# Performance work log

Hardware: AMD Instinct MI355X
Metric: run time of the kernel (lower is better)

## Reference

```python
import jax, jax.numpy as jnp
from jax import lax
import numpy as np

B, N, F_IN, T = 8, 2048, 2, 12
K, F_CHEV, F_TIME = 3, 64, 64
LN_EPS = 1e-5


def _cheb_polys(key):
    # random symmetric row-normalized 'scaled Laplacian' proxy, then Chebyshev recurrence
    A = jax.random.uniform(key, (N, N), dtype=jnp.float32)
    A = (A + A.T) * 0.5
    A = A / A.sum(axis=1, keepdims=True)
    L = A - jnp.eye(N, dtype=jnp.float32)  # eigenvalues roughly in [-1, 1]
    Ts = [jnp.eye(N, dtype=jnp.float32), L]
    for _ in range(2, K):
        Ts.append(2.0 * L @ Ts[-1] - Ts[-2])
    return jnp.stack(Ts[:K])  # (K, N, N)


def setup_inputs() -> dict:
    key = jax.random.key(0)
    ks = jax.random.split(key, 20)
    g = lambda i, s: jax.random.normal(ks[i], s, dtype=jnp.float32)
    xav = lambda i, s: g(i, s) * np.sqrt(2.0 / (s[-2] + s[-1]))
    return {
        "x": g(0, (B, N, F_IN, T)),
        "cheb": _cheb_polys(ks[1]),
        "Theta": xav(2, (K, F_IN, F_CHEV)),
        # temporal attention params
        "U1": g(3, (N,)), "U2": xav(4, (F_IN, N)), "U3": g(5, (F_IN,)),
        "be": g(6, (1, T, T)) * 0.1, "Ve": xav(7, (T, T)),
        # spatial attention params
        "W1": g(8, (T,)), "W2": xav(9, (F_IN, T)), "W3": g(10, (F_IN,)),
        "bs": g(11, (1, N, N)) * 0.1, "Vs": xav(12, (N, N)),
        # convs + layernorm
        "tconv_w": g(13, (F_TIME, F_CHEV, 1, 3)) * np.sqrt(2.0 / (F_CHEV * 3 + F_TIME)),
        "tconv_b": jax.random.uniform(ks[14], (F_TIME,), dtype=jnp.float32),
        "rconv_w": g(15, (F_TIME, F_IN, 1, 1)) * np.sqrt(2.0 / (F_IN + F_TIME)),
        "rconv_b": jax.random.uniform(ks[16], (F_TIME,), dtype=jnp.float32),
        "ln_g": jnp.ones((F_TIME,), jnp.float32),
        "ln_b": jnp.zeros((F_TIME,), jnp.float32),
    }


def _forward(x, cheb, Theta, U1, U2, U3, be, Ve, W1, W2, W3, bs, Vs,
             tconv_w, tconv_b, rconv_w, rconv_b, ln_g, ln_b):
    b, n, f, t = x.shape
    # ---- temporal attention: (B,T,T) ----
    lhs_t = jnp.einsum('bnft,n->btf', x, U1) @ U2          # (B,T,N)
    rhs_t = jnp.einsum('f,bnft->bnt', U3, x)               # (B,N,T)
    prod_t = jnp.einsum('btn,bnu->btu', lhs_t, rhs_t)      # (B,T,T)
    E = jnp.einsum('tu,buv->btv', Ve, jax.nn.sigmoid(prod_t + be))
    E = jax.nn.softmax(E, axis=1)
    # apply temporal attention
    x_TAt = (x.reshape(b, n * f, t) @ E).reshape(b, n, f, t)
    # ---- spatial attention: (B,N,N) ----
    lhs_s = jnp.einsum('bnft,t->bnf', x_TAt, W1) @ W2      # (B,N,T)
    rhs_s = jnp.einsum('f,bnft->btn', W3, x_TAt)           # (B,T,N)
    prod_s = jnp.einsum('bnt,btm->bnm', lhs_s, rhs_s)      # (B,N,N)
    S = jnp.einsum('mn,bnp->bmp', Vs, jax.nn.sigmoid(prod_s + bs))
    S = jax.nn.softmax(S, axis=1)
    # ---- Chebyshev graph conv with spatial attention (vectorized over k, t) ----
    # rhs[b,k,n,f,t] = sum_m (cheb[k,m,n] * S[b,m,n]) * x[b,m,f,t]
    rhs = jnp.einsum('kmn,bmn,bmft->bknft', cheb, S, x)
    gcn = jax.nn.relu(jnp.einsum('bknft,kfo->bnot', rhs, Theta))  # (B,N,F_chev,T)
    # ---- time conv (1x3, pad 1 along T) + 1x1 residual conv ----
    dn = ('NCHW', 'OIHW', 'NCHW')
    tc = lax.conv_general_dilated(gcn.transpose(0, 2, 1, 3), tconv_w, (1, 1),
                                  ((0, 0), (1, 1)), dimension_numbers=dn)
    tc = tc + tconv_b[None, :, None, None]                 # (B,F_time,N,T)
    res = lax.conv_general_dilated(x.transpose(0, 2, 1, 3), rconv_w, (1, 1),
                                   ((0, 0), (0, 0)), dimension_numbers=dn)
    res = res + rconv_b[None, :, None, None]
    y = jax.nn.relu(res + tc).transpose(0, 3, 2, 1)        # (B,T,N,F_time)
    mu = y.mean(-1, keepdims=True)
    var = jnp.mean((y - mu) ** 2, axis=-1, keepdims=True)
    y = (y - mu) * lax.rsqrt(var + LN_EPS) * ln_g + ln_b
    return y.transpose(0, 2, 3, 1)                          # (B,N,F_time,T)


def reference(x, cheb, Theta, U1, U2, U3, be, Ve, W1, W2, W3, bs, Vs,
              tconv_w, tconv_b, rconv_w, rconv_b, ln_g, ln_b):
    return _forward(x, cheb, Theta, U1, U2, U3, be, Ve, W1, W2, W3, bs, Vs,
                    tconv_w, tconv_b, rconv_w, rconv_b, ln_g, ln_b)
```

## Files before the change

kernel.cpp:

```cpp
#include <hip/hip_runtime.h>
#include <cstdint>
#include <cstddef>

#define NB 8
#define NN 2048
#define MCV 32

using bf16x8 = __attribute__((ext_vector_type(8))) __bf16;
using f32x4  = __attribute__((ext_vector_type(4))) float;

__device__ __forceinline__ float bf2f(unsigned short u) {
  union { unsigned int i; float f; } v; v.i = ((unsigned int)u) << 16; return v.f;
}
__device__ __forceinline__ unsigned short f2bf(float f) {
  union { float f; unsigned int i; } v; v.f = f;
  unsigned int lsb = (v.i >> 16) & 1u;
  v.i += 0x7fffu + lsb;
  return (unsigned short)(v.i >> 16);
}
__device__ __forceinline__ float ld_in(const void* p, size_t idx, int mode) {
  return mode ? bf2f(((const unsigned short*)p)[idx]) : ((const float*)p)[idx];
}
__device__ __forceinline__ int get_mode(const void* chebp) {
  return ((const unsigned int*)chebp)[0] != 0x3F800000u;
}

#define GLOAD16(gptr, lptr) \
  __builtin_amdgcn_global_load_lds((const __attribute__((address_space(1))) void*)(gptr), \
                                   (__attribute__((address_space(3))) void*)(lptr), 16, 0, 0)

struct Seg { const void* src; void* dst; int count; int tobf; };
struct ConvArgs { Seg s[16]; };

__global__ void k_convert(ConvArgs a, const void* __restrict__ chebp) {
  const int mode = get_mode(chebp);
  const int stride = gridDim.x * blockDim.x;
  for (int si = 0; si < 16; ++si) {
    const Seg sg = a.s[si];
    for (int i = blockIdx.x * blockDim.x + threadIdx.x; i < sg.count; i += stride) {
      float v = ld_in(sg.src, i, mode);
      if (sg.tobf) ((unsigned short*)sg.dst)[i] = f2bf(v);
      else         ((float*)sg.dst)[i] = v;
    }
  }
}

__global__ void k_vsb(const void* __restrict__ vs, unsigned short* __restrict__ out,
                      const void* __restrict__ tw, unsigned short* __restrict__ twr,
                      const void* __restrict__ chebp) {
  const int mode = get_mode(chebp);
  const int idx = blockIdx.x * 256 + threadIdx.x;
  if (idx < NN * NN) {
    const int ke = idx & 7, row = (idx >> 3) & 127, kc = (idx >> 10) & 7;
    const int hf = (idx >> 13) & 1, kt = (idx >> 14) & 31, mt = idx >> 19;
    const int m = mt * 256 + hf * 128 + row, k = kt * 64 + kc * 8 + ke;
    out[idx] = f2bf(ld_in(vs, (size_t)m * NN + k, mode));
  } else {
    const int j = idx - NN * NN;
    if (j < 12288) {
      const int dt = j >> 12, rem = j & 4095, o = rem >> 6, c = rem & 63;
      twr[j] = f2bf(ld_in(tw, (size_t)o * 192 + c * 3 + dt, mode));
    }
  }
}

__global__ __launch_bounds__(256) void k_temp1(const float* __restrict__ xf,
      const float* __restrict__ U1f, const float* __restrict__ U2f, const float* __restrict__ U3f,
      const float* __restrict__ bef, const float* __restrict__ Vef, float* __restrict__ E) {
  const int b = blockIdx.x;
  float accL[24], accG[24];
#pragma unroll
  for (int i = 0; i < 24; i++) { accL[i] = 0.f; accG[i] = 0.f; }
  const float u30 = U3f[0], u31 = U3f[1];
  for (int n = threadIdx.x; n < NN; n += 256) {
    const float* xp = xf + ((size_t)b * NN + n) * 24;
    const float u1 = U1f[n], u20 = U2f[n], u21 = U2f[NN + n];
#pragma unroll
    for (int t = 0; t < 12; t++) {
      float x0 = xp[t], x1 = xp[12 + t];
      accL[t * 2 + 0] += u1 * x0;
      accL[t * 2 + 1] += u1 * x1;
      float xs = u30 * x0 + u31 * x1;
      accG[t]      += u20 * xs;
      accG[12 + t] += u21 * xs;
    }
  }
#pragma unroll
  for (int i = 0; i < 24; i++) {
#pragma unroll
    for (int d = 32; d >= 1; d >>= 1) {
      accL[i] += __shfl_xor(accL[i], d, 64);
      accG[i] += __shfl_xor(accG[i], d, 64);
    }
  }
  __shared__ float red[4][48];
  __shared__ float L[48];
  __shared__ float s0[12][12], e1[12][12];
  const int lane = threadIdx.x & 63, wv = threadIdx.x >> 6;
  if (lane == 0) {
#pragma unroll
    for (int i = 0; i < 24; i++) { red[wv][i] = accL[i]; red[wv][24 + i] = accG[i]; }
  }
  __syncthreads();
  if (threadIdx.x < 48)
    L[threadIdx.x] = red[0][threadIdx.x] + red[1][threadIdx.x]
                   + red[2][threadIdx.x] + red[3][threadIdx.x];
  __syncthreads();
  const int tid = threadIdx.x;
  const int t = tid / 12, v = tid % 12;
  if (tid < 144) {
    float pr = L[t * 2 + 0] * L[24 + v] + L[t * 2 + 1] * L[36 + v] + bef[t * 12 + v];
    s0[t][v] = 1.f / (1.f + __expf(-pr));
  }
  __syncthreads();
  if (tid < 144) {
    float s = 0.f;
#pragma unroll
    for (int u = 0; u < 12; u++) s += Vef[t * 12 + u] * s0[u][v];
    e1[t][v] = s;
  }
  __syncthreads();
  if (tid < 144) {
    float mx = -1e30f;
#pragma unroll
    for (int u = 0; u < 12; u++) mx = fmaxf(mx, e1[u][v]);
    float sm = 0.f;
#pragma unroll
    for (int u = 0; u < 12; u++) sm += __expf(e1[u][v] - mx);
    E[b * 144 + t * 12 + v] = __expf(e1[t][v] - mx) / sm;
  }
}

__global__ __launch_bounds__(256) void k_xtat(const float* __restrict__ xf,
      const float* __restrict__ E, const float* __restrict__ W1f, const float* __restrict__ W2f,
      const float* __restrict__ W3f, float* __restrict__ lhs, float* __restrict__ rhsS) {
  const int b = blockIdx.y;
  const int n = blockIdx.x * 256 + threadIdx.x;
  __shared__ float Es[144];
  if (threadIdx.x < 144) Es[threadIdx.x] = E[b * 144 + threadIdx.x];
  __syncthreads();
  const float* xp = xf + ((size_t)b * NN + n) * 24;
  float xv[24];
#pragma unroll
  for (int i = 0; i < 24; i++) xv[i] = xp[i];
  float xT[24];
#pragma unroll
  for (int f = 0; f < 2; f++)
#pragma unroll
    for (int v = 0; v < 12; v++) {
      float s = 0.f;
#pragma unroll
      for (int u = 0; u < 12; u++) s += xv[f * 12 + u] * Es[u * 12 + v];
      xT[f * 12 + v] = s;
    }
  float a0 = 0.f, a1 = 0.f;
#pragma unroll
  for (int v = 0; v < 12; v++) { a0 += xT[v] * W1f[v]; a1 += xT[12 + v] * W1f[v]; }
  const float w30 = W3f[0], w31 = W3f[1];
  float* lp = lhs + ((size_t)b * NN + n) * 12;
#pragma unroll
  for (int t = 0; t < 12; t++) {
    lp[t] = a0 * W2f[t] + a1 * W2f[12 + t];
    rhsS[((size_t)b * 12 + t) * NN + n] = w30 * xT[t] + w31 * xT[12 + t];
  }
}

__global__ __launch_bounds__(256) void k_sig(const float* __restrict__ lhs,
      const float* __restrict__ rhsS, const void* __restrict__ bs,
      unsigned short* __restrict__ sigT, const void* __restrict__ chebp, int p0, int PL) {
  const int tid = threadIdx.x;
  const int n0 = blockIdx.x * 256;
  const int n = n0 + tid;
  const int pg0 = p0 + blockIdx.y * 16;
  const int mode = get_mode(chebp);
  __shared__ float rsl[8][12][16];
  __shared__ __align__(16) unsigned short sh[16][264];
  for (int i = tid; i < 1536; i += 256) {
    int b = i / 192, t = (i % 192) / 16, c = i % 16;
    rsl[b][t][c] = rhsS[((size_t)b * 12 + t) * NN + pg0 + c];
  }
  float bsv[16];
  if (mode) {
    const int4* bp = (const int4*)((const unsigned short*)bs + (size_t)n * NN + pg0);
    int4 q0 = bp[0], q1 = bp[1];
    const unsigned short* u0 = (const unsigned short*)&q0;
    const unsigned short* u1 = (const unsigned short*)&q1;
#pragma unroll
    for (int i = 0; i < 8; i++) { bsv[i] = bf2f(u0[i]); bsv[8 + i] = bf2f(u1[i]); }
  } else {
    const float4* fp = (const float4*)((const float*)bs + (size_t)n * NN + pg0);
#pragma unroll
    for (int q = 0; q < 4; q++) {
      float4 v = fp[q];
      bsv[q * 4 + 0] = v.x; bsv[q * 4 + 1] = v.y; bsv[q * 4 + 2] = v.z; bsv[q * 4 + 3] = v.w;
    }
  }
  __syncthreads();
  const int plbase = pg0 - p0;
  const size_t nbase = (size_t)(n0 >> 6) * 16384;
  for (int b = 0; b < 8; b++) {
    float lv[12];
    const float* lp = lhs + ((size_t)b * NN + n) * 12;
#pragma unroll
    for (int t = 0; t < 12; t++) lv[t] = lp[t];
#pragma unroll
    for (int pp = 0; pp < 16; pp++) {
      float acc = bsv[pp];
#pragma unroll
      for (int t = 0; t < 12; t++) acc += lv[t] * rsl[b][t][pp];
      float sg = 1.f / (1.f + __expf(-acc));
      sh[pp][tid] = f2bf(sg);
    }
    __syncthreads();
    const int gbase = b * PL + plbase;
    const size_t gt_off = (size_t)(gbase >> 8) * 524288 + (size_t)((gbase >> 7) & 1) * 8192
                        + (size_t)(gbase & 127) * 8 + nbase;
    for (int c = tid; c < 512; c += 256) {
      const int growL = c & 15, k3 = (c >> 4) & 7, n6 = c >> 7;
      int4 v = *(const int4*)&sh[growL][n6 * 64 + k3 * 8];
      *(int4*)&sigT[gt_off + (size_t)growL * 8 + (size_t)k3 * 1024 + (size_t)n6 * 16384] = v;
    }
    __syncthreads();
  }
}

__global__ __launch_bounds__(512, 2) void k_gemm(const unsigned short* __restrict__ A,
      const unsigned short* __restrict__ Bm, unsigned short* __restrict__ C,
      float* __restrict__ pmax, float* __restrict__ psum,
      int PL, int plshift, int GP, int nwg) {
  __shared__ __align__(16) unsigned short lA[2][16384];
  __shared__ __align__(16) unsigned short lB[2][16384];
  const int id = blockIdx.x;
  const int cpx = nwg >> 3;
  const int sid = (id & 7) * cpx + (id >> 3);
  const int s = sid >> 4, w = sid & 15;
  const int mt = (s & 1) * 4 + (w & 3);
  const int pt = (s >> 1) * 4 + (w >> 2);
  const int tid = threadIdx.x;
  const int wv = tid >> 6, lane = tid & 63;
  const int fr = lane & 15, hi = lane >> 4;
  const int wr = wv >> 2, wc = wv & 3;
  const unsigned short* gA = A  + (size_t)mt * 524288;
  const unsigned short* gB = Bm + (size_t)pt * 524288;

  f32x4 acc[8][4] = {};
  bf16x8 af[8][2], bfr[4][2];

#define STAGE_H(h) do { \
    const int kt_ = (h) >> 2, part_ = (h) & 3, r_ = part_ & 1; \
    const unsigned short* gsrc_ = ((part_ < 2) ? gA : gB) + (size_t)kt_ * 16384 + r_ * 8192 + tid * 8; \
    unsigned short* ldst_ = ((part_ < 2) ? &lA[0][0] : &lB[0][0]) + (kt_ & 1) * 16384 + r_ * 8192 + wv * 512; \
    GLOAD16(gsrc_,        ldst_); \
    GLOAD16(gsrc_ + 4096, ldst_ + 4096); \
  } while (0)

#define READ_A03(bf) do { \
    _Pragma("unroll") for (int mi_ = 0; mi_ < 4; ++mi_) \
    _Pragma("unroll") for (int s2_ = 0; s2_ < 2; ++s2_) \
      af[mi_][s2_] = *(const bf16x8*)&lA[bf][wr * 8192 + (s2_ * 4 + hi) * 1024 + (mi_ * 16 + fr) * 8]; \
  } while (0)

#define READ_A47(bf) do { \
    _Pragma("unroll") for (int mi_ = 4; mi_ < 8; ++mi_) \
    _Pragma("unroll") for (int s2_ = 0; s2_ < 2; ++s2_) \
      af[mi_][s2_] = *(const bf16x8*)&lA[bf][wr * 8192 + (s2_ * 4 + hi) * 1024 + (mi_ * 16 + fr) * 8]; \
  } while (0)

#define READ_B01(bf) do { \
    _Pragma("unroll") for (int ni_ = 0; ni_ < 2; ++ni_) \
    _Pragma("unroll") for (int s2_ = 0; s2_ < 2; ++s2_) \
      bfr[ni_][s2_] = *(const bf16x8*)&lB[bf][(wc >> 1) * 8192 + (s2_ * 4 + hi) * 1024 \
                                             + ((wc & 1) * 64 + ni_ * 16 + fr) * 8]; \
  } while (0)

#define READ_B23(bf) do { \
    _Pragma("unroll") for (int ni_ = 2; ni_ < 4; ++ni_) \
    _Pragma("unroll") for (int s2_ = 0; s2_ < 2; ++s2_) \
      bfr[ni_][s2_] = *(const bf16x8*)&lB[bf][(wc >> 1) * 8192 + (s2_ * 4 + hi) * 1024 \
                                             + ((wc & 1) * 64 + ni_ * 16 + fr) * 8]; \
  } while (0)

#define MFMA_Q(mh, nh) do { \
    __builtin_amdgcn_s_setprio(1); \
    _Pragma("unroll") for (int s2_ = 0; s2_ < 2; ++s2_) \
    _Pragma("unroll") for (int mi_ = 0; mi_ < 4; ++mi_) \
    _Pragma("unroll") for (int ni_ = 0; ni_ < 2; ++ni_) \
      acc[(mh) * 4 + mi_][(nh) * 2 + ni_] = __builtin_amdgcn_mfma_f32_16x16x32_bf16( \
          af[(mh) * 4 + mi_][s2_], bfr[(nh) * 2 + ni_][s2_], acc[(mh) * 4 + mi_][(nh) * 2 + ni_], 0, 0, 0); \
    __builtin_amdgcn_s_setprio(0); \
  } while (0)

#define PH_BAR() __builtin_amdgcn_s_barrier()
#define PH_LGKM() asm volatile("s_waitcnt lgkmcnt(0)" ::: "memory")

  for (int h = 0; h < 8; ++h) STAGE_H(h);
  asm volatile("s_waitcnt vmcnt(8)" ::: "memory");
  PH_BAR();

#pragma unroll 1
  for (int i = 0; i < 16; ++i) {
    const int hb = 8 * i;
    const bool more = (i < 15);
    READ_A03(0); READ_B01(0);
    if (i > 0) STAGE_H(hb + 4);
    PH_LGKM();
    MFMA_Q(0, 0);
    PH_BAR();
    READ_B23(0);
    if (i > 0) STAGE_H(hb + 5);
    PH_LGKM();
    MFMA_Q(0, 1);
    PH_BAR();
    READ_A47(0);
    if (more) STAGE_H(hb + 10);
    PH_LGKM();
    MFMA_Q(1, 0);
    PH_BAR();
    if (more) STAGE_H(hb + 11);
    MFMA_Q(1, 1);
    if (more) asm volatile("s_waitcnt vmcnt(4)" ::: "memory");
    else      asm volatile("s_waitcnt vmcnt(0)" ::: "memory");
    PH_BAR();
    READ_A03(1); READ_B01(1);
    if (more) STAGE_H(hb + 8);
    PH_LGKM();
    MFMA_Q(0, 0);
    PH_BAR();
    READ_B23(1);
    if (more) STAGE_H(hb + 9);
    PH_LGKM();
    MFMA_Q(0, 1);
    PH_BAR();
    READ_A47(1);
    if (more) STAGE_H(hb + 14);
    PH_LGKM();
    MFMA_Q(1, 0);
    PH_BAR();
    if (more) STAGE_H(hb + 15);
    MFMA_Q(1, 1);
    if (more) asm volatile("s_waitcnt vmcnt(4)" ::: "memory");
    else      asm volatile("s_waitcnt vmcnt(0)" ::: "memory");
    PH_BAR();
  }
#undef STAGE_H
#undef READ_A03
#undef READ_A47
#undef READ_B01
#undef READ_B23
#undef MFMA_Q
#undef PH_BAR
#undef PH_LGKM

  const int m0 = mt * 256, gcol0 = pt * 256;
  const int plmask = PL - 1;
#pragma unroll
  for (int ni = 0; ni < 4; ++ni) {
    float lmax = -1e30f;
    float vv[8][4];
#pragma unroll
    for (int mi = 0; mi < 8; ++mi)
#pragma unroll
      for (int r = 0; r < 4; r++) {
        float x = bf2f(f2bf(acc[mi][ni][r]));
        vv[mi][r] = x;
        lmax = fmaxf(lmax, x);
      }
    float lsum = 0.f;
#pragma unroll
    for (int mi = 0; mi < 8; ++mi)
#pragma unroll
      for (int r = 0; r < 4; r++) lsum += __expf(vv[mi][r] - lmax);
#pragma unroll
    for (int d = 16; d <= 32; d <<= 1) {
      float omax = __shfl_xor(lmax, d, 64);
      float osum = __shfl_xor(lsum, d, 64);
      float nm = fmaxf(lmax, omax);
      lsum = lsum * __expf(lmax - nm) + osum * __expf(omax - nm);
      lmax = nm;
    }
    if (hi == 0) {
      const int part = mt * 2 + wr;
      const int g = gcol0 + wc * 64 + ni * 16 + lane;
      pmax[(size_t)part * GP + g] = lmax;
      psum[(size_t)part * GP + g] = lsum;
    }
  }
#pragma unroll
  for (int mi = 0; mi < 8; ++mi) {
#pragma unroll
    for (int r = 0; r < 4; r++) {
      const int mrow = m0 + wr * 128 + mi * 16 + hi * 4 + r;
#pragma unroll
      for (int ni = 0; ni < 4; ++ni) {
        const int g = gcol0 + wc * 64 + ni * 16 + fr;
        const int b = g >> plshift, pl = g & plmask;
        C[((size_t)b * NN + mrow) * PL + pl] = f2bf(acc[mi][ni][r]);
      }
    }
  }
}

__global__ __launch_bounds__(256) void k_cheb(const unsigned short* __restrict__ S0c,
        const void* __restrict__ cheb, const unsigned short* __restrict__ cbf, int use_cbf,
        const float* __restrict__ xf, const float* __restrict__ pmax, const float* __restrict__ psum,
        unsigned short* __restrict__ part, int p0, int PL, int mspan, int GP) {
  const int b = blockIdx.z, mc = blockIdx.y;
  const int pl = blockIdx.x * 256 + threadIdx.x;
  const int n = p0 + pl;
  const int mode = get_mode(cheb);
  const int g = b * PL + pl;
  float mx = -1e30f;
#pragma unroll
  for (int c = 0; c < 16; c++) mx = fmaxf(mx, pmax[(size_t)c * GP + g]);
  float sm = 0.f;
#pragma unroll
  for (int c = 0; c < 16; c++) sm += psum[(size_t)c * GP + g] * __expf(pmax[(size_t)c * GP + g] - mx);
  const float inv = 1.f / sm;
  float acc[3][24];
#pragma unroll
  for (int k = 0; k < 3; k++)
#pragma unroll
    for (int j = 0; j < 24; j++) acc[k][j] = 0.f;
  const unsigned short* s0p = S0c + (size_t)b * NN * PL + pl;
  const int mEnd = mc * mspan + mspan;
  if (use_cbf || mode) {
    const unsigned short* cb = (use_cbf ? cbf : (const unsigned short*)cheb) + n;
#pragma unroll 2
    for (int m = mc * mspan; m < mEnd; ++m) {
      float w = __expf(bf2f(s0p[(size_t)m * PL]) - mx) * inv;
      const f32x4* xp = (const f32x4*)(xf + ((size_t)b * NN + m) * 24);
      float w0 = w * bf2f(cb[(size_t)m * NN]);
      float w1 = w * bf2f(cb[(size_t)NN * NN + (size_t)m * NN]);
      float w2 = w * bf2f(cb[(size_t)2 * NN * NN + (size_t)m * NN]);
#pragma unroll
      for (int q = 0; q < 6; q++) {
        f32x4 xv = xp[q];
#pragma unroll
        for (int e = 0; e < 4; e++) {
          int j = q * 4 + e;
          acc[0][j] += w0 * xv[e];
          acc[1][j] += w1 * xv[e];
          acc[2][j] += w2 * xv[e];
        }
      }
    }
  } else {
    const float* cb = (const float*)cheb + n;
#pragma unroll 2
    for (int m = mc * mspan; m < mEnd; ++m) {
      float w = __expf(bf2f(s0p[(size_t)m * PL]) - mx) * inv;
      const f32x4* xp = (const f32x4*)(xf + ((size_t)b * NN + m) * 24);
      float w0 = w * cb[(size_t)m * NN];
      float w1 = w * cb[(size_t)NN * NN + (size_t)m * NN];
      float w2 = w * cb[(size_t)2 * NN * NN + (size_t)m * NN];
#pragma unroll
      for (int q = 0; q < 6; q++) {
        f32x4 xv = xp[q];
#pragma unroll
        for (int e = 0; e < 4; e++) {
          int j = q * 4 + e;
          acc[0][j] += w0 * xv[e];
          acc[1][j] += w1 * xv[e];
          acc[2][j] += w2 * xv[e];
        }
      }
    }
  }
  unsigned short* pp = part + ((size_t)(mc * 8 + b) * 72) * PL + pl;
#pragma unroll
  for (int k = 0; k < 3; k++)
#pragma unroll
    for (int j = 0; j < 24; j++) pp[(size_t)(k * 24 + j) * PL] = f2bf(acc[k][j]);
}

__global__ void k_chebred(const unsigned short* __restrict__ part, float* __restrict__ rhsC,
                          int p0, int PL) {
  const int idx = blockIdx.x * 256 + threadIdx.x;
  if (idx >= 8 * 72 * PL) return;
  const int pl = idx % PL;
  const int r = idx / PL;
  const int j = r % 72, b = r / 72;
  float s = 0.f;
  for (int mc = 0; mc < MCV; ++mc)
    s += bf2f(part[((size_t)(mc * 8 + b) * 72 + j) * PL + pl]);
  rhsC[((size_t)b * NN + p0 + pl) * 72 + j] = s;
}

__global__ __launch_bounds__(256) void k_final(const float* __restrict__ rhsC,
      const float* __restrict__ Thf, const unsigned short* __restrict__ twr,
      const float* __restrict__ tbf, const float* __restrict__ rwf, const float* __restrict__ rbf,
      const float* __restrict__ lngf, const float* __restrict__ lnbf,
      const float* __restrict__ xf, void* __restrict__ out, const void* __restrict__ chebp) {
  const int mode = get_mode(chebp);
  __shared__ __align__(16) unsigned short ltw[192 * 72];
  __shared__ __align__(16) unsigned short gT[4][18][72];
  __shared__ float rl[4][72];
  __shared__ float prm[6][64];
  const int tid = threadIdx.x;
  const int wv = tid >> 6, lane = tid & 63;
  const size_t bn = (size_t)blockIdx.x * 4 + wv;

  for (int i = tid; i < 1536; i += 256) {
    const int row = i >> 3, cseg = (i & 7) * 8;
    *(bf16x8*)&ltw[row * 72 + cseg] = *(const bf16x8*)&twr[row * 64 + cseg];
  }
  if (tid < 64) {
    prm[0][tid] = tbf[tid] + rbf[tid];
    prm[1][tid] = rwf[tid * 2];
    prm[2][tid] = rwf[tid * 2 + 1];
    prm[3][tid] = lngf[tid];
    prm[4][tid] = lnbf[tid];
  }
  for (int i = lane; i < 648; i += 64) ((unsigned int*)&gT[wv][0][0])[i] = 0u;
  {
    const float* rp = rhsC + bn * 72;
    rl[wv][lane] = rp[lane];
    if (lane < 8) rl[wv][64 + lane] = rp[64 + lane];
  }
  __syncthreads();
  {
    const int c = lane;
    float th[6];
#pragma unroll
    for (int kf = 0; kf < 6; kf++) th[kf] = Thf[kf * 64 + c];
#pragma unroll
    for (int t = 0; t < 12; t++) {
      float s = 0.f;
#pragma unroll
      for (int kf = 0; kf < 6; kf++) s += rl[wv][kf * 12 + t] * th[kf];
      gT[wv][1 + t][c] = f2bf(fmaxf(s, 0.f));
    }
  }
  __syncthreads();
  const int fr = lane & 15, hi = lane >> 4;
  f32x4 acc4[4] = {};
#pragma unroll
  for (int dt = 0; dt < 3; dt++)
#pragma unroll
    for (int ks = 0; ks < 2; ks++) {
      bf16x8 bfrag = *(const bf16x8*)&gT[wv][fr + dt][ks * 32 + hi * 8];
#pragma unroll
      for (int ot = 0; ot < 4; ot++) {
        bf16x8 afrag = *(const bf16x8*)&ltw[(dt * 64 + ot * 16 + fr) * 72 + ks * 32 + hi * 8];
        acc4[ot] = __builtin_amdgcn_mfma_f32_16x16x32_bf16(afrag, bfrag, acc4[ot], 0, 0, 0);
      }
    }
  const int t = fr;
  const int tc = t < 12 ? t : 11;
  const float x0 = xf[bn * 24 + tc], x1 = xf[bn * 24 + 12 + tc];
  float vals[4][4];
  float sum = 0.f, sumsq = 0.f;
#pragma unroll
  for (int ot = 0; ot < 4; ot++) {
    f32x4 rbt4 = *(const f32x4*)&prm[0][ot * 16 + hi * 4];
    f32x4 rw04 = *(const f32x4*)&prm[1][ot * 16 + hi * 4];
    f32x4 rw14 = *(const f32x4*)&prm[2][ot * 16 + hi * 4];
#pragma unroll
    for (int r = 0; r < 4; r++) {
      float v = acc4[ot][r] + rbt4[r] + rw04[r] * x0 + rw14[r] * x1;
      v = fmaxf(v, 0.f);
      vals[ot][r] = v;
      sum += v; sumsq += v * v;
    }
  }
  sum   += __shfl_xor(sum, 16, 64);
  sumsq += __shfl_xor(sumsq, 16, 64);
  sum   += __shfl_xor(sum, 32, 64);
  sumsq += __shfl_xor(sumsq, 32, 64);
  const float mu = sum * (1.f / 64.f);
  const float var = sumsq * (1.f / 64.f) - mu * mu;
  const float rs = rsqrtf(var + 1e-5f);
  if (t < 12) {
#pragma unroll
    for (int ot = 0; ot < 4; ot++) {
      f32x4 lg4 = *(const f32x4*)&prm[3][ot * 16 + hi * 4];
      f32x4 lb4 = *(const f32x4*)&prm[4][ot * 16 + hi * 4];
#pragma unroll
      for (int r = 0; r < 4; r++) {
        const int o = ot * 16 + hi * 4 + r;
        float y = (vals[ot][r] - mu) * rs * lg4[r] + lb4[r];
        if (mode) ((unsigned short*)out)[bn * 768 + o * 12 + t] = f2bf(y);
        else      ((float*)out)[bn * 768 + o * 12 + t] = y;
      }
    }
  }
}

struct Plan {
  size_t o_xf, o_Th, o_U1, o_U2, o_U3, o_be, o_Ve, o_W1, o_W2, o_W3,
         o_twr, o_tb, o_rw, o_rb, o_lg, o_lb, o_Vs,
         o_E, o_lhs, o_rhsS, o_rhsC,
         o_R1, o_S0, o_pmax, o_psum, o_cbf;
  size_t total;
};

static Plan make_plan(int PL, int cbf) {
  Plan p; size_t off = 0;
  auto al = [&](size_t b) { size_t r = off; off += (b + 255) & ~(size_t)255; return r; };
  const int GP = 8 * PL;
  p.o_xf   = al((size_t)NB * NN * 24 * 4);
  p.o_Th   = al(384 * 4);
  p.o_U1   = al(2048 * 4);
  p.o_U2   = al(4096 * 4);
  p.o_U3   = al(2 * 4);
  p.o_be   = al(144 * 4);
  p.o_Ve   = al(144 * 4);
  p.o_W1   = al(12 * 4);
  p.o_W2   = al(24 * 4);
  p.o_W3   = al(2 * 4);
  p.o_twr  = al(12288 * 2);
  p.o_tb   = al(64 * 4);
  p.o_rw   = al(128 * 4);
  p.o_rb   = al(64 * 4);
  p.o_lg   = al(64 * 4);
  p.o_lb   = al(64 * 4);
  p.o_Vs   = al((size_t)NN * NN * 2);
  p.o_E    = al(NB * 144 * 4);
  p.o_lhs  = al((size_t)NB * NN * 12 * 4);
  p.o_rhsS = al((size_t)NB * 12 * NN * 4);
  p.o_rhsC = al((size_t)NB * NN * 72 * 4);
  p.o_R1   = al((size_t)36864 * PL);
  p.o_S0   = al((size_t)NB * NN * PL * 2);
  p.o_pmax = al((size_t)16 * GP * 4);
  p.o_psum = al((size_t)16 * GP * 4);
  p.o_cbf  = cbf ? al((size_t)3 * NN * NN * 2) : 0;
  p.total = off;
  return p;
}

extern "C" void kernel_launch(void* const* d_in, const int* in_sizes, int n_in,
                              void* d_out, int out_size, void* d_ws, size_t ws_size,
                              hipStream_t stream) {
  (void)in_sizes; (void)n_in; (void)out_size;
  char* ws = (char*)d_ws;

  int PL, use_cbf;
  if      (make_plan(1024, 1).total <= ws_size) { PL = 1024; use_cbf = 1; }
  else if (make_plan(1024, 0).total <= ws_size) { PL = 1024; use_cbf = 0; }
  else if (make_plan(512, 1).total  <= ws_size) { PL = 512;  use_cbf = 1; }
  else                                          { PL = 512;  use_cbf = 0; }
  const Plan P = make_plan(PL, use_cbf);
  const int GP = 8 * PL;
  const int plshift = (PL == 512) ? 9 : 10;
  const int mspan = NN / MCV;
  const void* chebp = d_in[1];

  float* xf   = (float*)(ws + P.o_xf);
  float* Ebuf = (float*)(ws + P.o_E);
  float* lhs  = (float*)(ws + P.o_lhs);
  float* rhsS = (float*)(ws + P.o_rhsS);
  float* rhsC = (float*)(ws + P.o_rhsC);
  unsigned short* sigT = (unsigned short*)(ws + P.o_R1);
  unsigned short* part = (unsigned short*)(ws + P.o_R1);
  unsigned short* S0c  = (unsigned short*)(ws + P.o_S0);
  float* pmax = (float*)(ws + P.o_pmax);
  float* psum = (float*)(ws + P.o_psum);
  unsigned short* cbfp = use_cbf ? (unsigned short*)(ws + P.o_cbf)
                                 : (unsigned short*)d_in[1];

  ConvArgs ca;
  auto seg = [&](int i, int di, size_t o, int count, int tobf) {
    ca.s[i].src = d_in[di]; ca.s[i].dst = (void*)(ws + o); ca.s[i].count = count; ca.s[i].tobf = tobf;
  };
  seg(0, 0, P.o_xf, 393216, 0);
  seg(1, 2, P.o_Th, 384, 0);
  seg(2, 3, P.o_U1, 2048, 0);
  seg(3, 4, P.o_U2, 4096, 0);
  seg(4, 5, P.o_U3, 2, 0);
  seg(5, 6, P.o_be, 144, 0);
  seg(6, 7, P.o_Ve, 144, 0);
  seg(7, 8, P.o_W1, 12, 0);
  seg(8, 9, P.o_W2, 24, 0);
  seg(9, 10, P.o_W3, 2, 0);
  seg(10, 14, P.o_tb, 64, 0);
  seg(11, 15, P.o_rw, 128, 0);
  seg(12, 16, P.o_rb, 64, 0);
  seg(13, 17, P.o_lg, 64, 0);
  seg(14, 18, P.o_lb, 64, 0);
  seg(15, 1, P.o_cbf, use_cbf ? 3 * NN * NN : 0, 1);
  k_convert<<<1024, 256, 0, stream>>>(ca, chebp);
  k_vsb<<<(NN * NN + 12288 + 255) / 256, 256, 0, stream>>>(d_in[12],
      (unsigned short*)(ws + P.o_Vs), d_in[13], (unsigned short*)(ws + P.o_twr), chebp);

  k_temp1<<<NB, 256, 0, stream>>>(xf, (float*)(ws + P.o_U1), (float*)(ws + P.o_U2),
                                  (float*)(ws + P.o_U3), (float*)(ws + P.o_be),
                                  (float*)(ws + P.o_Ve), Ebuf);
  k_xtat<<<dim3(8, NB), 256, 0, stream>>>(xf, Ebuf, (float*)(ws + P.o_W1), (float*)(ws + P.o_W2),
                                          (float*)(ws + P.o_W3), lhs, rhsS);

  const int nwg = 8 * (GP / 256);
  for (int p0 = 0; p0 < NN; p0 += PL) {
    k_sig<<<dim3(8, PL / 16), 256, 0, stream>>>(lhs, rhsS, d_in[11], sigT, chebp, p0, PL);
    k_gemm<<<nwg, 512, 0, stream>>>((unsigned short*)(ws + P.o_Vs), sigT, S0c,
                                    pmax, psum, PL, plshift, GP, nwg);
    k_cheb<<<dim3(PL / 256, MCV, NB), 256, 0, stream>>>(S0c, d_in[1], cbfp, use_cbf,
                                                        xf, pmax, psum, part, p0, PL, mspan, GP);
    k_chebred<<<(8 * 72 * PL + 255) / 256, 256, 0, stream>>>(part, rhsC, p0, PL);
  }

  k_final<<<NB * NN / 4, 256, 0, stream>>>(rhsC, (float*)(ws + P.o_Th),
      (unsigned short*)(ws + P.o_twr), (float*)(ws + P.o_tb), (float*)(ws + P.o_rw),
      (float*)(ws + P.o_rb), (float*)(ws + P.o_lg), (float*)(ws + P.o_lb), xf, d_out, chebp);
}
```

Baseline: 348.1 us.

## Shrink GEMM tile to 128x256 with K-step 32 for higher occupancy

The Vs×sigmoid GEMM now uses 128-row M tiles and 32-wide K steps instead of 256x256 tiles with K-step 64. LDS buffers shrink, launch bounds allow 4 workgroups per CU, and twice as many workgroups are launched. The Vs and sigT pre-layouts, the staging schedule and the partial softmax max/sum reduction (now 32 partials) are all adjusted to match. The aim is better occupancy and CU fill, at the cost of less data reuse per tile and more barriers and LDS traffic per FLOP.

Measured after the change: 357.7 us. 1.03x slower.

```diff
diff --git a/kernel.cpp b/kernel.cpp
--- a/kernel.cpp
+++ b/kernel.cpp
@@ -51,9 +51,9 @@
   const int mode = get_mode(chebp);
   const int idx = blockIdx.x * 256 + threadIdx.x;
   if (idx < NN * NN) {
-    const int ke = idx & 7, row = (idx >> 3) & 127, kc = (idx >> 10) & 7;
-    const int hf = (idx >> 13) & 1, kt = (idx >> 14) & 31, mt = idx >> 19;
-    const int m = mt * 256 + hf * 128 + row, k = kt * 64 + kc * 8 + ke;
+    const int ke = idx & 7, row = (idx >> 3) & 127, kc = (idx >> 10) & 3;
+    const int kt = (idx >> 12) & 63, mt = idx >> 18;
+    const int m = mt * 128 + row, k = kt * 32 + kc * 8 + ke;
     out[idx] = f2bf(ld_in(vs, (size_t)m * NN + k, mode));
   } else {
     const int j = idx - NN * NN;
@@ -197,7 +197,7 @@
   }
   __syncthreads();
   const int plbase = pg0 - p0;
-  const size_t nbase = (size_t)(n0 >> 6) * 16384;
+  const size_t nbase = (size_t)(n0 >> 5) * 8192;
   for (int b = 0; b < 8; b++) {
     float lv[12];
     const float* lp = lhs + ((size_t)b * NN + n) * 12;
@@ -213,152 +213,142 @@
     }
     __syncthreads();
     const int gbase = b * PL + plbase;
-    const size_t gt_off = (size_t)(gbase >> 8) * 524288 + (size_t)((gbase >> 7) & 1) * 8192
+    const size_t gt_off = (size_t)(gbase >> 8) * 524288 + (size_t)((gbase >> 7) & 1) * 4096
                         + (size_t)(gbase & 127) * 8 + nbase;
     for (int c = tid; c < 512; c += 256) {
-      const int growL = c & 15, k3 = (c >> 4) & 7, n6 = c >> 7;
-      int4 v = *(const int4*)&sh[growL][n6 * 64 + k3 * 8];
-      *(int4*)&sigT[gt_off + (size_t)growL * 8 + (size_t)k3 * 1024 + (size_t)n6 * 16384] = v;
+      const int growL = c & 15, lchunk = c >> 4;
+      int4 v = *(const int4*)&sh[growL][lchunk * 8];
+      *(int4*)&sigT[gt_off + (size_t)growL * 8 + (size_t)(lchunk & 3) * 1024
+                    + (size_t)(lchunk >> 2) * 8192] = v;
     }
     __syncthreads();
   }
 }
 
-__global__ __launch_bounds__(512, 2) void k_gemm(const unsigned short* __restrict__ A,
+__global__ __launch_bounds__(512, 4) void k_gemm(const unsigned short* __restrict__ A,
       const unsigned short* __restrict__ Bm, unsigned short* __restrict__ C,
       float* __restrict__ pmax, float* __restrict__ psum,
       int PL, int plshift, int GP, int nwg) {
-  __shared__ __align__(16) unsigned short lA[2][16384];
-  __shared__ __align__(16) unsigned short lB[2][16384];
+  __shared__ __align__(16) unsigned short lA[2][4096];
+  __shared__ __align__(16) unsigned short lB[2][8192];
   const int id = blockIdx.x;
   const int cpx = nwg >> 3;
   const int sid = (id & 7) * cpx + (id >> 3);
   const int s = sid >> 4, w = sid & 15;
-  const int mt = (s & 1) * 4 + (w & 3);
-  const int pt = (s >> 1) * 4 + (w >> 2);
+  const int mt = (s & 3) * 4 + (w & 3);
+  const int pt = (s >> 2) * 4 + (w >> 2);
   const int tid = threadIdx.x;
   const int wv = tid >> 6, lane = tid & 63;
   const int fr = lane & 15, hi = lane >> 4;
   const int wr = wv >> 2, wc = wv & 3;
-  const unsigned short* gA = A  + (size_t)mt * 524288;
+  const unsigned short* gA = A  + (size_t)mt * 262144;
   const unsigned short* gB = Bm + (size_t)pt * 524288;
 
-  f32x4 acc[8][4] = {};
-  bf16x8 af[8][2], bfr[4][2];
-
-#define STAGE_H(h) do { \
-    const int kt_ = (h) >> 2, part_ = (h) & 3, r_ = part_ & 1; \
-    const unsigned short* gsrc_ = ((part_ < 2) ? gA : gB) + (size_t)kt_ * 16384 + r_ * 8192 + tid * 8; \
-    unsigned short* ldst_ = ((part_ < 2) ? &lA[0][0] : &lB[0][0]) + (kt_ & 1) * 16384 + r_ * 8192 + wv * 512; \
-    GLOAD16(gsrc_,        ldst_); \
-    GLOAD16(gsrc_ + 4096, ldst_ + 4096); \
+  f32x4 acc[4][4] = {};
+  bf16x8 af[4], bfr[4];
+
+#define STAGE_A(kt) GLOAD16(gA + (size_t)(kt) * 4096 + tid * 8, \
+                            &lA[0][0] + ((kt) & 1) * 4096 + wv * 512)
+#define STAGE_B(kt, r) GLOAD16(gB + (size_t)(kt) * 8192 + (r) * 4096 + tid * 8, \
+                               &lB[0][0] + ((kt) & 1) * 8192 + (r) * 4096 + wv * 512)
+
+#define READ_A01(bf) do { \
+    _Pragma("unroll") for (int mi_ = 0; mi_ < 2; ++mi_) \
+      af[mi_] = *(const bf16x8*)&lA[bf][hi * 1024 + (wr * 64 + mi_ * 16 + fr) * 8]; \
   } while (0)
-
-#define READ_A03(bf) do { \
-    _Pragma("unroll") for (int mi_ = 0; mi_ < 4; ++mi_) \
-    _Pragma("unroll") for (int s2_ = 0; s2_ < 2; ++s2_) \
-      af[mi_][s2_] = *(const bf16x8*)&lA[bf][wr * 8192 + (s2_ * 4 + hi) * 1024 + (mi_ * 16 + fr) * 8]; \
+#define READ_A23(bf) do { \
+    _Pragma("unroll") for (int mi_ = 2; mi_ < 4; ++mi_) \
+      af[mi_] = *(const bf16x8*)&lA[bf][hi * 1024 + (wr * 64 + mi_ * 16 + fr) * 8]; \
   } while (0)
-
-#define READ_A47(bf) do { \
-    _Pragma("unroll") for (int mi_ = 4; mi_ < 8; ++mi_) \
-    _Pragma("unroll") for (int s2_ = 0; s2_ < 2; ++s2_) \
-      af[mi_][s2_] = *(const bf16x8*)&lA[bf][wr * 8192 + (s2_ * 4 + hi) * 1024 + (mi_ * 16 + fr) * 8]; \
-  } while (0)
-
 #define READ_B01(bf) do { \
     _Pragma("unroll") for (int ni_ = 0; ni_ < 2; ++ni_) \
-    _Pragma("unroll") for (int s2_ = 0; s2_ < 2; ++s2_) \
-      bfr[ni_][s2_] = *(const bf16x8*)&lB[bf][(wc >> 1) * 8192 + (s2_ * 4 + hi) * 1024 \
-                                             + ((wc & 1) * 64 + ni_ * 16 + fr) * 8]; \
+      bfr[ni_] = *(const bf16x8*)&lB[bf][(wc >> 1) * 4096 + hi * 1024 \
+                                         + ((wc & 1) * 64 + ni_ * 16 + fr) * 8]; \
   } while (0)
-
 #define READ_B23(bf) do { \
     _Pragma("unroll") for (int ni_ = 2; ni_ < 4; ++ni_) \
-    _Pragma("unroll") for (int s2_ = 0; s2_ < 2; ++s2_) \
-      bfr[ni_][s2_] = *(const bf16x8*)&lB[bf][(wc >> 1) * 8192 + (s2_ * 4 + hi) * 1024 \
-                                             + ((wc & 1) * 64 + ni_ * 16 + fr) * 8]; \
+      bfr[ni_] = *(const bf16x8*)&lB[bf][(wc >> 1) * 4096 + hi * 1024 \
+                                         + ((wc & 1) * 64 + ni_ * 16 + fr) * 8]; \
   } while (0)
 
 #define MFMA_Q(mh, nh) do { \
     __builtin_amdgcn_s_setprio(1); \
-    _Pragma("unroll") for (int s2_ = 0; s2_ < 2; ++s2_) \
-    _Pragma("unroll") for (int mi_ = 0; mi_ < 4; ++mi_) \
+    _Pragma("unroll") for (int mi_ = 0; mi_ < 2; ++mi_) \
     _Pragma("unroll") for (int ni_ = 0; ni_ < 2; ++ni_) \
-      acc[(mh) * 4 + mi_][(nh) * 2 + ni_] = __builtin_amdgcn_mfma_f32_16x16x32_bf16( \
-          af[(mh) * 4 + mi_][s2_], bfr[(nh) * 2 + ni_][s2_], acc[(mh) * 4 + mi_][(nh) * 2 + ni_], 0, 0, 0); \
+      acc[(mh) * 2 + mi_][(nh) * 2 + ni_] = __builtin_amdgcn_mfma_f32_16x16x32_bf16( \
+          af[(mh) * 2 + mi_], bfr[(nh) * 2 + ni_], acc[(mh) * 2 + mi_][(nh) * 2 + ni_], 0, 0, 0); \
     __builtin_amdgcn_s_setprio(0); \
   } while (0)
 
 #define PH_BAR() __builtin_amdgcn_s_barrier()
 #define PH_LGKM() asm volatile("s_waitcnt lgkmcnt(0)" ::: "memory")
 
-  for (int h = 0; h < 8; ++h) STAGE_H(h);
-  asm volatile("s_waitcnt vmcnt(8)" ::: "memory");
+  STAGE_A(0); STAGE_B(0, 0); STAGE_B(0, 1);
+  STAGE_A(1); STAGE_B(1, 0); STAGE_B(1, 1);
+  asm volatile("s_waitcnt vmcnt(3)" ::: "memory");
   PH_BAR();
 
 #pragma unroll 1
-  for (int i = 0; i < 16; ++i) {
-    const int hb = 8 * i;
-    const bool more = (i < 15);
-    READ_A03(0); READ_B01(0);
-    if (i > 0) STAGE_H(hb + 4);
+  for (int i = 0; i < 32; ++i) {
+    const int t0 = 2 * i, t1 = 2 * i + 1;
+    const bool more = (i < 31);
+    READ_A01(0); READ_B01(0);
+    if (i > 0) STAGE_A(t1);
     PH_LGKM();
     MFMA_Q(0, 0);
     PH_BAR();
     READ_B23(0);
-    if (i > 0) STAGE_H(hb + 5);
     PH_LGKM();
     MFMA_Q(0, 1);
     PH_BAR();
-    READ_A47(0);
-    if (more) STAGE_H(hb + 10);
+    READ_A23(0);
+    if (more) STAGE_B(t0 + 2, 0);
     PH_LGKM();
     MFMA_Q(1, 0);
     PH_BAR();
-    if (more) STAGE_H(hb + 11);
+    if (more) STAGE_B(t0 + 2, 1);
     MFMA_Q(1, 1);
-    if (more) asm volatile("s_waitcnt vmcnt(4)" ::: "memory");
+    if (more) asm volatile("s_waitcnt vmcnt(2)" ::: "memory");
     else      asm volatile("s_waitcnt vmcnt(0)" ::: "memory");
     PH_BAR();
-    READ_A03(1); READ_B01(1);
-    if (more) STAGE_H(hb + 8);
+    READ_A01(1); READ_B01(1);
+    if (more) STAGE_A(t0 + 2);
     PH_LGKM();
     MFMA_Q(0, 0);
     PH_BAR();
     READ_B23(1);
-    if (more) STAGE_H(hb + 9);
     PH_LGKM();
     MFMA_Q(0, 1);
     PH_BAR();
-    READ_A47(1);
-    if (more) STAGE_H(hb + 14);
+    READ_A23(1);
+    if (more) STAGE_B(t1 + 2, 0);
     PH_LGKM();
     MFMA_Q(1, 0);
     PH_BAR();
-    if (more) STAGE_H(hb + 15);
+    if (more) STAGE_B(t1 + 2, 1);
     MFMA_Q(1, 1);
-    if (more) asm volatile("s_waitcnt vmcnt(4)" ::: "memory");
+    if (more) asm volatile("s_waitcnt vmcnt(2)" ::: "memory");
     else      asm volatile("s_waitcnt vmcnt(0)" ::: "memory");
     PH_BAR();
   }
-#undef STAGE_H
-#undef READ_A03
-#undef READ_A47
+#undef STAGE_A
+#undef STAGE_B
+#undef READ_A01
+#undef READ_A23
 #undef READ_B01
 #undef READ_B23
 #undef MFMA_Q
 #undef PH_BAR
 #undef PH_LGKM
 
-  const int m0 = mt * 256, gcol0 = pt * 256;
+  const int m0 = mt * 128, gcol0 = pt * 256;
   const int plmask = PL - 1;
 #pragma unroll
   for (int ni = 0; ni < 4; ++ni) {
     float lmax = -1e30f;
-    float vv[8][4];
-#pragma unroll
-    for (int mi = 0; mi < 8; ++mi)
+    float vv[4][4];
+#pragma unroll
+    for (int mi = 0; mi < 4; ++mi)
 #pragma unroll
       for (int r = 0; r < 4; r++) {
         float x = bf2f(f2bf(acc[mi][ni][r]));
@@ -367,7 +357,7 @@
       }
     float lsum = 0.f;
 #pragma unroll
-    for (int mi = 0; mi < 8; ++mi)
+    for (int mi = 0; mi < 4; ++mi)
 #pragma unroll
       for (int r = 0; r < 4; r++) lsum += __expf(vv[mi][r] - lmax);
 #pragma unroll
@@ -386,10 +376,10 @@
     }
   }
 #pragma unroll
-  for (int mi = 0; mi < 8; ++mi) {
+  for (int mi = 0; mi < 4; ++mi) {
 #pragma unroll
     for (int r = 0; r < 4; r++) {
-      const int mrow = m0 + wr * 128 + mi * 16 + hi * 4 + r;
+      const int mrow = m0 + wr * 64 + mi * 16 + hi * 4 + r;
 #pragma unroll
       for (int ni = 0; ni < 4; ++ni) {
         const int g = gcol0 + wc * 64 + ni * 16 + fr;
@@ -411,10 +401,10 @@
   const int g = b * PL + pl;
   float mx = -1e30f;
 #pragma unroll
-  for (int c = 0; c < 16; c++) mx = fmaxf(mx, pmax[(size_t)c * GP + g]);
+  for (int c = 0; c < 32; c++) mx = fmaxf(mx, pmax[(size_t)c * GP + g]);
   float sm = 0.f;
 #pragma unroll
-  for (int c = 0; c < 16; c++) sm += psum[(size_t)c * GP + g] * __expf(pmax[(size_t)c * GP + g] - mx);
+  for (int c = 0; c < 32; c++) sm += psum[(size_t)c * GP + g] * __expf(pmax[(size_t)c * GP + g] - mx);
   const float inv = 1.f / sm;
   float acc[3][24];
 #pragma unroll
@@ -621,8 +611,8 @@
   p.o_rhsC = al((size_t)NB * NN * 72 * 4);
   p.o_R1   = al((size_t)36864 * PL);
   p.o_S0   = al((size_t)NB * NN * PL * 2);
-  p.o_pmax = al((size_t)16 * GP * 4);
-  p.o_psum = al((size_t)16 * GP * 4);
+  p.o_pmax = al((size_t)32 * GP * 4);
+  p.o_psum = al((size_t)32 * GP * 4);
   p.o_cbf  = cbf ? al((size_t)3 * NN * NN * 2) : 0;
   p.total = off;
   return p;
@@ -688,7 +678,7 @@
   k_xtat<<<dim3(8, NB), 256, 0, stream>>>(xf, Ebuf, (float*)(ws + P.o_W1), (float*)(ws + P.o_W2),
                                           (float*)(ws + P.o_W3), lhs, rhsS);
 
-  const int nwg = 8 * (GP / 256);
+  const int nwg = 16 * (GP / 256);
   for (int p0 = 0; p0 < NN; p0 += PL) {
     k_sig<<<dim3(8, PL / 16), 256, 0, stream>>>(lhs, rhsS, d_in[11], sigT, chebp, p0, PL);
     k_gemm<<<nwg, 512, 0, stream>>>((unsigned short*)(ws + P.o_Vs), sigT, S0c,
```
